# Kernel optimization log

Measured on AMD Instinct MI355X. Metric: run time of the kernel, lower is better.

## Reference

```python
import jax, jax.numpy as jnp
import numpy as np

B, N, D, K = 4, 4096, 2048, 4  # batch, seq_len, hidden_size, conv_kernel


def setup_inputs() -> dict:
    key = jax.random.key(0)
    k1, k2, k3 = jax.random.split(key, 3)
    x = jax.random.normal(k1, (B, N, D), dtype=jnp.float32)
    conv_weight = jax.random.normal(k2, (D, K), dtype=jnp.float32) * 0.1  # depthwise weight [D, K]
    conv_bias = jax.random.normal(k3, (D,), dtype=jnp.float32) * 0.1
    return {"x": x, "conv_weight": conv_weight, "conv_bias": conv_bias}


def reference(x, conv_weight, conv_bias):
    # Prefill path of TTTConv: depthwise causal conv1d + cache-state extraction.
    Bx, Nx, Dx = x.shape
    Kx = conv_weight.shape[1]
    xt = jnp.transpose(x, (0, 2, 1))  # [B, D, N]
    kernel = conv_weight[:, None, :]  # [D, 1, K] (O, I/groups, K)
    y = jax.lax.conv_general_dilated(
        xt, kernel,
        window_strides=(1,),
        padding=[(Kx - 1, 0)],  # causal left pad only (causal_conv1d_fn semantics)
        dimension_numbers=("NCH", "OIH", "NCH"),
        feature_group_count=Dx,
    )
    y = y + conv_bias[None, :, None]
    conv_output = jnp.transpose(y, (0, 2, 1))  # [B, N, D]
    # cache state: F.pad(x^T, (K - N, 0)) with N >= K crops to the last K timesteps
    conv_states = xt[:, :, Nx - Kx:]  # [B, D, K]
    return conv_output, conv_states
```

## Files before the change

### kernel.cpp

```cpp
#include <hip/hip_runtime.h>


constexpr int B = 4, N = 4096, D = 2048, K = 4;
constexpr int T = 16;
constexpr int BLK = 256;
constexpr int DV = D / 4;
constexpr int DBLKS = DV / BLK;
constexpr int NCHUNKS = N / T;

typedef float v4f __attribute__((ext_vector_type(4)));

__global__ __launch_bounds__(BLK) void tttconv_fused(
    const float* __restrict__ x, const float* __restrict__ w,
    const float* __restrict__ bias, float* __restrict__ out,
    float* __restrict__ st)
{
    int bid = blockIdx.x;
    int b = bid / (NCHUNKS * DBLKS);
    int rem = bid % (NCHUNKS * DBLKS);
    int nchunk = rem / DBLKS;
    int dblk = rem % DBLKS;
    int dv = dblk * BLK + threadIdx.x;
    int d = dv * 4;
    int n0 = nchunk * T;

    const float4* w4 = (const float4*)(w + (size_t)d * K);
    float4 wr0 = w4[0];
    float4 wr1 = w4[1];
    float4 wr2 = w4[2];
    float4 wr3 = w4[3];
    float4 bv = *(const float4*)(bias + d);

    const float* xbase = x + ((size_t)b * N) * D + d;
    float4 xin[T + K - 1];
    if (n0 >= K - 1) {
        #pragma unroll
        for (int j = 0; j < T + K - 1; ++j)
            xin[j] = *(const float4*)(xbase + (size_t)(n0 - (K - 1) + j) * D);
    } else {
        #pragma unroll
        for (int j = 0; j < T + K - 1; ++j) {
            int n = n0 - (K - 1) + j;
            xin[j] = (n >= 0) ? *(const float4*)(xbase + (size_t)n * D)
                              : make_float4(0.f, 0.f, 0.f, 0.f);
        }
    }

    float* obase = out + ((size_t)b * N) * D + d;
    #pragma unroll
    for (int t = 0; t < T; ++t) {
        float4 acc = bv;
        acc.x += wr0.x * xin[t + 0].x + wr0.y * xin[t + 1].x + wr0.z * xin[t + 2].x + wr0.w * xin[t + 3].x;
        acc.y += wr1.x * xin[t + 0].y + wr1.y * xin[t + 1].y + wr1.z * xin[t + 2].y + wr1.w * xin[t + 3].y;
        acc.z += wr2.x * xin[t + 0].z + wr2.y * xin[t + 1].z + wr2.z * xin[t + 2].z + wr2.w * xin[t + 3].z;
        acc.w += wr3.x * xin[t + 0].w + wr3.y * xin[t + 1].w + wr3.z * xin[t + 2].w + wr3.w * xin[t + 3].w;
        v4f av = { acc.x, acc.y, acc.z, acc.w };
        __builtin_nontemporal_store(av, (v4f*)(obase + (size_t)(n0 + t) * D));
    }

    if (nchunk == NCHUNKS - 1) {
        float4* stp = (float4*)(st + ((size_t)b * D + d) * K);
        stp[0] = make_float4(xin[T - 1].x, xin[T].x, xin[T + 1].x, xin[T + 2].x);
        stp[1] = make_float4(xin[T - 1].y, xin[T].y, xin[T + 1].y, xin[T + 2].y);
        stp[2] = make_float4(xin[T - 1].z, xin[T].z, xin[T + 1].z, xin[T + 2].z);
        stp[3] = make_float4(xin[T - 1].w, xin[T].w, xin[T + 1].w, xin[T + 2].w);
    }
}

extern "C" void kernel_launch(void* const* d_in, const int* in_sizes, int n_in,
                              void* d_out, int out_size, void* d_ws, size_t ws_size,
                              hipStream_t stream)
{
    const float* x    = (const float*)d_in[0];
    const float* w    = (const float*)d_in[1];
    const float* bias = (const float*)d_in[2];
    float* out = (float*)d_out;
    float* st  = out + (size_t)B * N * D;

    tttconv_fused<<<B * NCHUNKS * DBLKS, BLK, 0, stream>>>(x, w, bias, out, st);
}
```

Before: 239.7 us.

## Restructure conv to full-row blocks with sliding window and XCD swizzle

Each block now processes all channels of a row for eight consecutive timesteps, keeping a three-row sliding window in registers and loading each new row inside the loop. Block indices are swizzled across the eight XCDs so that neighbouring time chunks land on the same die's L2, where halo rows can be reused. Output stores are plain instead of nontemporal. Smaller chunks raise the relative cost of halo rereads, and interleaving loads with compute may reduce how many loads are in flight.

```diff
diff --git a/kernel.cpp b/kernel.cpp
--- a/kernel.cpp
+++ b/kernel.cpp
@@ -2,68 +2,80 @@
 
 
 constexpr int B = 4, N = 4096, D = 2048, K = 4;
-constexpr int T = 16;
+constexpr int Tb = 8;
+constexpr int NB = N / Tb;
 constexpr int BLK = 256;
-constexpr int DV = D / 4;
-constexpr int DBLKS = DV / BLK;
-constexpr int NCHUNKS = N / T;
+constexpr int GRID = B * NB;
 
-typedef float v4f __attribute__((ext_vector_type(4)));
-
-__global__ __launch_bounds__(BLK) void tttconv_fused(
+__global__ __launch_bounds__(BLK) void tttconv_stream(
     const float* __restrict__ x, const float* __restrict__ w,
     const float* __restrict__ bias, float* __restrict__ out,
     float* __restrict__ st)
 {
-    int bid = blockIdx.x;
-    int b = bid / (NCHUNKS * DBLKS);
-    int rem = bid % (NCHUNKS * DBLKS);
-    int nchunk = rem / DBLKS;
-    int dblk = rem % DBLKS;
-    int dv = dblk * BLK + threadIdx.x;
-    int d = dv * 4;
-    int n0 = nchunk * T;
+    int lb = (blockIdx.x & 7) * (GRID / 8) + (blockIdx.x >> 3);
+    int b  = lb / NB;
+    int nc = lb % NB;
+    int n0 = nc * Tb;
+    int tid = threadIdx.x;
+    int d0 = tid * 4;
+    int d1 = d0 + 1024;
 
-    const float4* w4 = (const float4*)(w + (size_t)d * K);
-    float4 wr0 = w4[0];
-    float4 wr1 = w4[1];
-    float4 wr2 = w4[2];
-    float4 wr3 = w4[3];
-    float4 bv = *(const float4*)(bias + d);
+    const float4* w4 = (const float4*)w;
+    float4 wa0 = w4[d0], wa1 = w4[d0 + 1], wa2 = w4[d0 + 2], wa3 = w4[d0 + 3];
+    float4 wb0 = w4[d1], wb1 = w4[d1 + 1], wb2 = w4[d1 + 2], wb3 = w4[d1 + 3];
+    float4 bva = *(const float4*)(bias + d0);
+    float4 bvb = *(const float4*)(bias + d1);
 
-    const float* xbase = x + ((size_t)b * N) * D + d;
-    float4 xin[T + K - 1];
-    if (n0 >= K - 1) {
-        #pragma unroll
-        for (int j = 0; j < T + K - 1; ++j)
-            xin[j] = *(const float4*)(xbase + (size_t)(n0 - (K - 1) + j) * D);
+    const float* xb = x + ((size_t)b * N) * D;
+    float* ob = out + ((size_t)b * N) * D;
+
+    float4 a0, a1, a2, c0, c1, c2;
+    if (nc > 0) {
+        a0 = *(const float4*)(xb + (size_t)(n0 - 3) * D + d0);
+        c0 = *(const float4*)(xb + (size_t)(n0 - 3) * D + d1);
+        a1 = *(const float4*)(xb + (size_t)(n0 - 2) * D + d0);
+        c1 = *(const float4*)(xb + (size_t)(n0 - 2) * D + d1);
+        a2 = *(const float4*)(xb + (size_t)(n0 - 1) * D + d0);
+        c2 = *(const float4*)(xb + (size_t)(n0 - 1) * D + d1);
     } else {
-        #pragma unroll
-        for (int j = 0; j < T + K - 1; ++j) {
-            int n = n0 - (K - 1) + j;
-            xin[j] = (n >= 0) ? *(const float4*)(xbase + (size_t)n * D)
-                              : make_float4(0.f, 0.f, 0.f, 0.f);
-        }
+        a0 = a1 = a2 = make_float4(0.f, 0.f, 0.f, 0.f);
+        c0 = c1 = c2 = a0;
     }
 
-    float* obase = out + ((size_t)b * N) * D + d;
     #pragma unroll
-    for (int t = 0; t < T; ++t) {
-        float4 acc = bv;
-        acc.x += wr0.x * xin[t + 0].x + wr0.y * xin[t + 1].x + wr0.z * xin[t + 2].x + wr0.w * xin[t + 3].x;
-        acc.y += wr1.x * xin[t + 0].y + wr1.y * xin[t + 1].y + wr1.z * xin[t + 2].y + wr1.w * xin[t + 3].y;
-        acc.z += wr2.x * xin[t + 0].z + wr2.y * xin[t + 1].z + wr2.z * xin[t + 2].z + wr2.w * xin[t + 3].z;
-        acc.w += wr3.x * xin[t + 0].w + wr3.y * xin[t + 1].w + wr3.z * xin[t + 2].w + wr3.w * xin[t + 3].w;
-        v4f av = { acc.x, acc.y, acc.z, acc.w };
-        __builtin_nontemporal_store(av, (v4f*)(obase + (size_t)(n0 + t) * D));
-    }
+    for (int t = 0; t < Tb; ++t) {
+        size_t roff = (size_t)(n0 + t) * D;
+        float4 ca = *(const float4*)(xb + roff + d0);
+        float4 cb = *(const float4*)(xb + roff + d1);
 
-    if (nchunk == NCHUNKS - 1) {
-        float4* stp = (float4*)(st + ((size_t)b * D + d) * K);
-        stp[0] = make_float4(xin[T - 1].x, xin[T].x, xin[T + 1].x, xin[T + 2].x);
-        stp[1] = make_float4(xin[T - 1].y, xin[T].y, xin[T + 1].y, xin[T + 2].y);
-        stp[2] = make_float4(xin[T - 1].z, xin[T].z, xin[T + 1].z, xin[T + 2].z);
-        stp[3] = make_float4(xin[T - 1].w, xin[T].w, xin[T + 1].w, xin[T + 2].w);
+        float4 oa, oc;
+        oa.x = bva.x + wa0.x * a0.x + wa0.y * a1.x + wa0.z * a2.x + wa0.w * ca.x;
+        oa.y = bva.y + wa1.x * a0.y + wa1.y * a1.y + wa1.z * a2.y + wa1.w * ca.y;
+        oa.z = bva.z + wa2.x * a0.z + wa2.y * a1.z + wa2.z * a2.z + wa2.w * ca.z;
+        oa.w = bva.w + wa3.x * a0.w + wa3.y * a1.w + wa3.z * a2.w + wa3.w * ca.w;
+        oc.x = bvb.x + wb0.x * c0.x + wb0.y * c1.x + wb0.z * c2.x + wb0.w * cb.x;
+        oc.y = bvb.y + wb1.x * c0.y + wb1.y * c1.y + wb1.z * c2.y + wb1.w * cb.y;
+        oc.z = bvb.z + wb2.x * c0.z + wb2.y * c1.z + wb2.z * c2.z + wb2.w * cb.z;
+        oc.w = bvb.w + wb3.x * c0.w + wb3.y * c1.w + wb3.z * c2.w + wb3.w * cb.w;
+
+        *(float4*)(ob + roff + d0) = oa;
+        *(float4*)(ob + roff + d1) = oc;
+
+        if (t == Tb - 1 && nc == NB - 1) {
+            float4* sa = (float4*)(st + ((size_t)b * D + d0) * K);
+            sa[0] = make_float4(a0.x, a1.x, a2.x, ca.x);
+            sa[1] = make_float4(a0.y, a1.y, a2.y, ca.y);
+            sa[2] = make_float4(a0.z, a1.z, a2.z, ca.z);
+            sa[3] = make_float4(a0.w, a1.w, a2.w, ca.w);
+            float4* sb = (float4*)(st + ((size_t)b * D + d1) * K);
+            sb[0] = make_float4(c0.x, c1.x, c2.x, cb.x);
+            sb[1] = make_float4(c0.y, c1.y, c2.y, cb.y);
+            sb[2] = make_float4(c0.z, c1.z, c2.z, cb.z);
+            sb[3] = make_float4(c0.w, c1.w, c2.w, cb.w);
+        }
+
+        a0 = a1; a1 = a2; a2 = ca;
+        c0 = c1; c1 = c2; c2 = cb;
     }
 }
 
@@ -77,5 +89,5 @@
     float* out = (float*)d_out;
     float* st  = out + (size_t)B * N * D;
 
-    tttconv_fused<<<B * NCHUNKS * DBLKS, BLK, 0, stream>>>(x, w, bias, out, st);
+    tttconv_stream<<<GRID, BLK, 0, stream>>>(x, w, bias, out, st);
 }
```

Result: slower. 252.5 us (+5.4%).
